# Kernel tuning notes

Hardware: AMD Instinct MI355X
Metric: run time of the kernel (lower is better)

Reference implementation:

```python
import jax, jax.numpy as jnp
import numpy as np

N, E = 50000, 1600000
IN, OUT, H = 128, 32, 2
NT, ET = 20, 4
ETE, EAE, ED = 16, 16, 16
SLOPE = 0.2  # conv_neg_slope


def setup_inputs() -> dict:
    key = jax.random.key(0)
    ks = jax.random.split(key, 11)
    d_att = 2 * OUT + ETE + EAE
    return dict(
        x=jax.random.normal(ks[0], (N, IN), jnp.float32),
        edge_index=jax.random.randint(ks[1], (2, E), 0, N),
        ntypes=jax.random.randint(ks[2], (N,), 0, NT),
        etypes=jax.random.randint(ks[3], (E,), 0, ET),
        eattr=jax.random.normal(ks[4], (E, ED), jnp.float32),
        het_W=jax.random.normal(ks[5], (NT, IN, OUT), jnp.float32) / np.sqrt(IN).astype(np.float32),
        het_b=jnp.zeros((NT, OUT), jnp.float32),
        etype_table=jax.random.normal(ks[6], (ET, ETE), jnp.float32),
        eattr_W=jax.random.normal(ks[7], (ED, EAE), jnp.float32) / np.sqrt(ED).astype(np.float32),
        att_W=jax.random.normal(ks[8], (d_att, H), jnp.float32) / np.sqrt(d_att).astype(np.float32),
        lin_W=jax.random.normal(ks[9], (OUT + EAE, OUT), jnp.float32) / np.sqrt(OUT + EAE).astype(np.float32),
    )


def _lrelu(v):
    return jax.nn.leaky_relu(v, SLOPE)


def _heat_conv(x, edge_index, ntypes, etypes, eattr,
               het_W, het_b, etype_table, eattr_W, att_W, lin_W):
    # HeteroLinear: node-type-conditioned linear transform (loop over 20 types,
    # avoids materializing a [N, IN, OUT] gathered-weight tensor)
    h = jnp.zeros((x.shape[0], het_W.shape[-1]), x.dtype)
    for t in range(het_W.shape[0]):
        h = h + jnp.where((ntypes == t)[:, None], x @ het_W[t] + het_b[t], 0.0)

    src, dst = edge_index[0], edge_index[1]
    ete = _lrelu(etype_table[etypes])        # [E, ETE] edge-type embedding
    ea = _lrelu(eattr @ eattr_W)             # [E, EAE] edge-attr embedding
    x_i = h[dst]                             # target node feats [E, OUT]
    x_j = h[src]                             # source node feats [E, OUT]

    feat = jnp.concatenate([x_i, x_j, ete, ea], axis=-1)
    alpha = _lrelu(feat @ att_W)             # [E, H] raw attention logits

    # softmax grouped by destination node, per head
    amax = jax.ops.segment_max(alpha, dst, num_segments=N)  # [N, H]
    alpha = jnp.exp(alpha - amax[dst])
    denom = jax.ops.segment_sum(alpha, dst, num_segments=N)  # [N, H]
    alpha = alpha / denom[dst]

    msg = jnp.concatenate([x_j, ea], axis=-1) @ lin_W        # [E, OUT]
    m = (msg[:, None, :] * alpha[:, :, None]).reshape(alpha.shape[0], H * OUT)
    out = jax.ops.segment_sum(m, dst, num_segments=N)        # [N, H*OUT]
    return out  # concat=True -> flattened heads


def reference(x, edge_index, ntypes, etypes, eattr,
              het_W, het_b, etype_table, eattr_W, att_W, lin_W):
    out = _heat_conv(x, edge_index, ntypes, etypes, eattr,
                     het_W, het_b, etype_table, eattr_W, att_W, lin_W)
    return jax.nn.relu(out)  # final activation in forward (eval mode: no dropout)
```

## Files before the change

kernel.cpp:

```cpp
#include <hip/hip_runtime.h>
#include <hip/hip_fp16.h>

#define NN 50000
#define EE 1600000
#define IN_F 128
#define SLOPE 0.2f
#define NB_SCAN 196
#define NSHARD 8

typedef _Float16 hf2 __attribute__((ext_vector_type(2)));

__global__ __launch_bounds__(256) void k_node(
    const float* __restrict__ x, const int* __restrict__ ntypes,
    const float* __restrict__ hetW, const float* __restrict__ hetb,
    const float* __restrict__ linW, const float* __restrict__ attW,
    float* __restrict__ hlin, float* __restrict__ auxS,
    float* __restrict__ auxD)
{
    __shared__ float sH[32 * 33];
    __shared__ float sLin[32 * 32];
    int tid = threadIdx.x;
    for (int i = tid; i < 1024; i += 256) sLin[i] = linW[i];

    int g = tid >> 3;
    int j = tid & 7;
    int n = blockIdx.x * 32 + g;
    int nc = n < NN ? n : NN - 1;
    int t = ntypes[nc];
    const float* W = hetW + (size_t)t * (IN_F * 32);
    const float4* xr = (const float4*)(x + (size_t)nc * IN_F);

    float4 acc = ((const float4*)(hetb + t * 32))[j];
    #pragma unroll 4
    for (int c = 0; c < 32; ++c) {
        float4 xv = xr[c];
        const float* Wr = W + (4 * c) * 32 + 4 * j;
        float4 w0 = *(const float4*)(Wr);
        float4 w1 = *(const float4*)(Wr + 32);
        float4 w2 = *(const float4*)(Wr + 64);
        float4 w3 = *(const float4*)(Wr + 96);
        acc.x += xv.x * w0.x + xv.y * w1.x + xv.z * w2.x + xv.w * w3.x;
        acc.y += xv.x * w0.y + xv.y * w1.y + xv.z * w2.y + xv.w * w3.y;
        acc.z += xv.x * w0.z + xv.y * w1.z + xv.z * w2.z + xv.w * w3.z;
        acc.w += xv.x * w0.w + xv.y * w1.w + xv.z * w2.w + xv.w * w3.w;
    }
    sH[g * 33 + 4 * j + 0] = acc.x;
    sH[g * 33 + 4 * j + 1] = acc.y;
    sH[g * 33 + 4 * j + 2] = acc.z;
    sH[g * 33 + 4 * j + 3] = acc.w;
    __syncthreads();

    int o = tid & 31;
    #pragma unroll
    for (int pass = 0; pass < 4; ++pass) {
        int g2 = (tid >> 5) + 8 * pass;
        int n2 = blockIdx.x * 32 + g2;
        if (n2 >= NN) break;
        float accl = 0.0f;
        #pragma unroll
        for (int k = 0; k < 32; ++k)
            accl += sH[g2 * 33 + k] * sLin[k * 32 + o];
        hlin[(size_t)n2 * 32 + o] = accl;

        float hv = sH[g2 * 33 + o];
        float p0 = hv * attW[o * 2],        p1 = hv * attW[o * 2 + 1];
        float p2 = hv * attW[(32 + o) * 2], p3 = hv * attW[(32 + o) * 2 + 1];
        #pragma unroll
        for (int m = 16; m >= 1; m >>= 1) {
            p0 += __shfl_xor(p0, m, 32);
            p1 += __shfl_xor(p1, m, 32);
            p2 += __shfl_xor(p2, m, 32);
            p3 += __shfl_xor(p3, m, 32);
        }
        if (o == 0) {
            auxD[n2 * 2] = p0; auxD[n2 * 2 + 1] = p1;
            auxS[n2 * 2] = p2; auxS[n2 * 2 + 1] = p3;
        }
    }
}

__global__ __launch_bounds__(256) void k_count(
    const int* __restrict__ dst, int* __restrict__ cnt8,
    unsigned* __restrict__ rankpack)
{
    int e = blockIdx.x * 256 + threadIdx.x;
    int d = dst[e];
    unsigned xcc;
    asm volatile("s_getreg_b32 %0, hwreg(HW_REG_XCC_ID)" : "=s"(xcc));
    int sh = xcc & (NSHARD - 1);
    int lr = atomicAdd(&cnt8[sh * NN + d], 1);
    rankpack[e] = ((unsigned)lr << 3) | (unsigned)sh;
}

__global__ __launch_bounds__(256) void k_scanA(
    const int* __restrict__ cnt8, int* __restrict__ offsets,
    int* __restrict__ bsum, int* __restrict__ sb8)
{
    __shared__ int s[256];
    int t = threadIdx.x;
    int i = blockIdx.x * 256 + t;
    int tot = 0;
    if (i < NN) {
        int pre = 0;
        #pragma unroll
        for (int sh = 0; sh < NSHARD; ++sh) {
            int c = cnt8[sh * NN + i];
            sb8[sh * NN + i] = pre;
            pre += c;
        }
        tot = pre;
    }
    s[t] = tot;
    __syncthreads();
    for (int off = 1; off < 256; off <<= 1) {
        int v = (t >= off) ? s[t - off] : 0;
        __syncthreads();
        s[t] += v;
        __syncthreads();
    }
    if (i < NN) offsets[i] = s[t] - tot;
    if (t == 255) bsum[blockIdx.x] = s[255];
}

__global__ __launch_bounds__(256) void k_scanB(
    const int* __restrict__ bsum, int* __restrict__ bbase,
    const float* __restrict__ etab, const float* __restrict__ attW,
    float* __restrict__ etedot)
{
    __shared__ int s[256];
    int t = threadIdx.x;
    if (t < 8) {
        int et = t >> 1, hh = t & 1;
        float acc = 0.0f;
        for (int k = 0; k < 16; ++k) {
            float v = etab[et * 16 + k];
            v = v > 0.0f ? v : SLOPE * v;
            acc += v * attW[(64 + k) * 2 + hh];
        }
        etedot[t] = acc;
    }
    int c = (t < NB_SCAN) ? bsum[t] : 0;
    s[t] = c;
    __syncthreads();
    for (int off = 1; off < 256; off <<= 1) {
        int v = (t >= off) ? s[t - off] : 0;
        __syncthreads();
        s[t] += v;
        __syncthreads();
    }
    if (t < NB_SCAN) bbase[t] = s[t] - c;
}

__global__ __launch_bounds__(256) void k_scanC(
    int* __restrict__ offsets, const int* __restrict__ bbase,
    int* __restrict__ sb8)
{
    int t = threadIdx.x;
    int i = blockIdx.x * 256 + t;
    if (i < NN) {
        int v = offsets[i] + bbase[blockIdx.x];
        offsets[i] = v;
        #pragma unroll
        for (int sh = 0; sh < NSHARD; ++sh)
            sb8[sh * NN + i] += v;
    }
    if (i == 0) offsets[NN] = EE;
}

__global__ __launch_bounds__(256) void k_pre6(
    const int* __restrict__ srcp, const int* __restrict__ dstp,
    const int* __restrict__ etypes, const float* __restrict__ eattr,
    const float* __restrict__ eaW, const float* __restrict__ attW,
    const float* __restrict__ etedot, const float* __restrict__ auxS,
    const float* __restrict__ auxD, const unsigned* __restrict__ rankpack,
    const int* __restrict__ sb8, float4* __restrict__ recBuf)
{
    int e = blockIdx.x * 256 + threadIdx.x;
    int s = srcp[e], d = dstp[e], et = etypes[e];
    unsigned rp = rankpack[e];
    int slot = sb8[(size_t)(rp & 7) * NN + d] + (int)(rp >> 3);

    float attr[16];
    {
        const float4* ap = (const float4*)(eattr + (size_t)e * 16);
        #pragma unroll
        for (int q = 0; q < 4; ++q) {
            float4 v = ap[q];
            attr[4*q+0] = v.x; attr[4*q+1] = v.y;
            attr[4*q+2] = v.z; attr[4*q+3] = v.w;
        }
    }
    float ea[16];
    #pragma unroll
    for (int j = 0; j < 16; ++j) {
        float acc = 0.0f;
        #pragma unroll
        for (int k = 0; k < 16; ++k) acc += attr[k] * eaW[k * 16 + j];
        ea[j] = acc > 0.0f ? acc : SLOPE * acc;
    }

    float2 aD = ((const float2*)auxD)[d];
    float2 aS = ((const float2*)auxS)[s];
    float2 eD = ((const float2*)etedot)[et];
    float al0 = aD.x + aS.x + eD.x;
    float al1 = aD.y + aS.y + eD.y;
    #pragma unroll
    for (int j = 0; j < 16; ++j) {
        al0 += ea[j] * attW[(80 + j) * 2];
        al1 += ea[j] * attW[(80 + j) * 2 + 1];
    }
    al0 = al0 > 0.0f ? al0 : SLOPE * al0;
    al1 = al1 > 0.0f ? al1 : SLOPE * al1;
    float p0 = __expf(al0), p1 = __expf(al1);

    __half2 eh[8];
    #pragma unroll
    for (int q = 0; q < 8; ++q)
        eh[q] = __floats2half2_rn(ea[2*q], ea[2*q+1]);

    float4* P = recBuf + (size_t)slot * 4;
    P[0] = ((const float4*)eh)[0];
    P[1] = ((const float4*)eh)[1];
    union { float4 v; int i[4]; float f[4]; } mu;
    mu.i[0] = s; mu.f[1] = p0; mu.f[2] = p1; mu.i[3] = 0;
    P[2] = mu.v;
    P[3] = make_float4(0.f, 0.f, 0.f, 0.f);
}

__global__ __launch_bounds__(256) void k_gather5(
    const int* __restrict__ offsets, const float4* __restrict__ recBuf,
    const float* __restrict__ hlin, const float* __restrict__ linW,
    float* __restrict__ out)
{
    int tid = blockIdx.x * 256 + threadIdx.x;
    int n = tid >> 6;
    int lane = threadIdx.x & 63;
    if (n >= NN) return;
    int o = lane & 31, hh = lane >> 5, j = o & 15;

    int s0 = __builtin_amdgcn_readfirstlane(offsets[n]);
    int s1 = __builtin_amdgcn_readfirstlane(offsets[n + 1]);

    const char* base = (const char*)recBuf;
    float accm = 0.0f, accp = 0.0f, wacc = 0.0f;

    int slot = s0;
    for (; slot + 3 < s1; slot += 4) {
        const char* r0 = base + ((size_t)(slot + 0) << 6);
        const char* r1 = base + ((size_t)(slot + 1) << 6);
        const char* r2 = base + ((size_t)(slot + 2) << 6);
        const char* r3 = base + ((size_t)(slot + 3) << 6);
        int4 m0 = *(const int4*)(r0 + 32);
        int4 m1 = *(const int4*)(r1 + 32);
        int4 m2 = *(const int4*)(r2 + 32);
        int4 m3 = *(const int4*)(r3 + 32);
        float e0 = __half2float(*(const __half*)(r0 + 2 * j));
        float e1 = __half2float(*(const __half*)(r1 + 2 * j));
        float e2 = __half2float(*(const __half*)(r2 + 2 * j));
        float e3 = __half2float(*(const __half*)(r3 + 2 * j));
        float hv0 = hlin[(size_t)m0.x * 32 + o];
        float hv1 = hlin[(size_t)m1.x * 32 + o];
        float hv2 = hlin[(size_t)m2.x * 32 + o];
        float hv3 = hlin[(size_t)m3.x * 32 + o];
        float p0 = __int_as_float(hh ? m0.z : m0.y);
        float p1 = __int_as_float(hh ? m1.z : m1.y);
        float p2 = __int_as_float(hh ? m2.z : m2.y);
        float p3 = __int_as_float(hh ? m3.z : m3.y);
        accm += p0 * hv0;
        accm += p1 * hv1;
        accm += p2 * hv2;
        accm += p3 * hv3;
        wacc += p0 * e0;
        wacc += p1 * e1;
        wacc += p2 * e2;
        wacc += p3 * e3;
        accp += (p0 + p1) + (p2 + p3);
    }
    for (; slot < s1; ++slot) {
        const char* r = base + ((size_t)slot << 6);
        int4 m = *(const int4*)(r + 32);
        float e = __half2float(*(const __half*)(r + 2 * j));
        float hv = hlin[(size_t)m.x * 32 + o];
        float p = __int_as_float(hh ? m.z : m.y);
        accm += p * hv;
        wacc += p * e;
        accp += p;
    }

    float elin = 0.0f;
    int bsel = lane & 32;
    #pragma unroll
    for (int jj = 0; jj < 16; ++jj) {
        float wv = __shfl(wacc, bsel | jj, 64);
        elin += wv * linW[(32 + jj) * 32 + o];
    }
    float num = accm + elin;
    float v = accp > 0.0f ? num / accp : 0.0f;
    out[(size_t)n * 64 + lane] = v > 0.0f ? v : 0.0f;
}

extern "C" void kernel_launch(void* const* d_in, const int* in_sizes, int n_in,
                              void* d_out, int out_size, void* d_ws, size_t ws_size,
                              hipStream_t stream)
{
    const float* x      = (const float*)d_in[0];
    const int*   eidx   = (const int*)  d_in[1];
    const int*   ntypes = (const int*)  d_in[2];
    const int*   etypes = (const int*)  d_in[3];
    const float* eattr  = (const float*)d_in[4];
    const float* hetW   = (const float*)d_in[5];
    const float* hetb   = (const float*)d_in[6];
    const float* etab   = (const float*)d_in[7];
    const float* eaW    = (const float*)d_in[8];
    const float* attW   = (const float*)d_in[9];
    const float* linW   = (const float*)d_in[10];
    float* out = (float*)d_out;

    char* ws = (char*)d_ws;
    size_t off = 0;
    auto alloc = [&](size_t bytes) {
        char* p = ws + off;
        off = (off + bytes + 255) & ~(size_t)255;
        return p;
    };
    float*    hlin     = (float*)   alloc((size_t)NN * 32 * sizeof(float));
    float*    auxS     = (float*)   alloc((size_t)NN * 2 * sizeof(float));
    float*    auxD     = (float*)   alloc((size_t)NN * 2 * sizeof(float));
    float*    etedot   = (float*)   alloc(8 * sizeof(float));
    int*      cnt8     = (int*)     alloc((size_t)NSHARD * NN * sizeof(int));
    int*      offsets  = (int*)     alloc(((size_t)NN + 1) * sizeof(int));
    int*      sb8      = (int*)     alloc((size_t)NSHARD * NN * sizeof(int));
    unsigned* rankpack = (unsigned*)alloc((size_t)EE * sizeof(unsigned));
    int*      bsum     = (int*)     alloc(256 * sizeof(int));
    int*      bbase    = (int*)     alloc(256 * sizeof(int));
    float4*   recBuf   = (float4*)  alloc((size_t)EE * 64);
    (void)ws_size;

    const int* srcp = eidx;
    const int* dstp = eidx + EE;

    hipMemsetAsync(cnt8, 0, (size_t)NSHARD * NN * sizeof(int), stream);

    k_node<<<(NN + 31) / 32, 256, 0, stream>>>(x, ntypes, hetW, hetb, linW,
                                               attW, hlin, auxS, auxD);
    k_count<<<EE / 256, 256, 0, stream>>>(dstp, cnt8, rankpack);
    k_scanA<<<NB_SCAN, 256, 0, stream>>>(cnt8, offsets, bsum, sb8);
    k_scanB<<<1, 256, 0, stream>>>(bsum, bbase, etab, attW, etedot);
    k_scanC<<<NB_SCAN, 256, 0, stream>>>(offsets, bbase, sb8);
    k_pre6<<<EE / 256, 256, 0, stream>>>(srcp, dstp, etypes, eattr, eaW, attW,
                                         etedot, auxS, auxD, rankpack, sb8,
                                         recBuf);
    k_gather5<<<(NN * 64 + 255) / 256, 256, 0, stream>>>(offsets, recBuf,
                                                         hlin, linW, out);
}
```

Baseline: 464.6 us.

## Fuse node transform with edge counting and store projected node features in fp16

The node HeteroLinear kernel and the per-destination atomic counting kernel become one launch. Every fifth block does node work and the other blocks do edge counting, so the compute-bound and atomic-bound work can overlap and one launch is saved. The lin_W-projected node features (hlin) are now written and read as fp16, which halves the bytes of the random per-edge gathers in the final aggregation kernel. The cost is reduced precision on the node message features.

Result: faster. 454.3 us (-2.2%).

```diff
diff --git a/kernel.cpp b/kernel.cpp
--- a/kernel.cpp
+++ b/kernel.cpp
@@ -7,24 +7,42 @@
 #define SLOPE 0.2f
 #define NB_SCAN 196
 #define NSHARD 8
+#define NB_NODE 1563
+#define NB_CNT  6250
+#define NB_FUSE (NB_NODE + NB_CNT)
 
 typedef _Float16 hf2 __attribute__((ext_vector_type(2)));
 
-__global__ __launch_bounds__(256) void k_node(
+__global__ __launch_bounds__(256) void k_node_count(
     const float* __restrict__ x, const int* __restrict__ ntypes,
     const float* __restrict__ hetW, const float* __restrict__ hetb,
     const float* __restrict__ linW, const float* __restrict__ attW,
-    float* __restrict__ hlin, float* __restrict__ auxS,
-    float* __restrict__ auxD)
-{
+    __half* __restrict__ hlinH, float* __restrict__ auxS,
+    float* __restrict__ auxD,
+    const int* __restrict__ dst, int* __restrict__ cnt8,
+    unsigned* __restrict__ rankpack)
+{
+    int b = blockIdx.x;
+    int tid = threadIdx.x;
+    if (b % 5 != 0) {
+        int cid = b - b / 5 - 1;
+        int e = cid * 256 + tid;
+        int d = dst[e];
+        unsigned xcc;
+        asm volatile("s_getreg_b32 %0, hwreg(HW_REG_XCC_ID)" : "=s"(xcc));
+        int sh = xcc & (NSHARD - 1);
+        int lr = atomicAdd(&cnt8[sh * NN + d], 1);
+        rankpack[e] = ((unsigned)lr << 3) | (unsigned)sh;
+        return;
+    }
+    int nb = b / 5;
     __shared__ float sH[32 * 33];
     __shared__ float sLin[32 * 32];
-    int tid = threadIdx.x;
     for (int i = tid; i < 1024; i += 256) sLin[i] = linW[i];
 
     int g = tid >> 3;
     int j = tid & 7;
-    int n = blockIdx.x * 32 + g;
+    int n = nb * 32 + g;
     int nc = n < NN ? n : NN - 1;
     int t = ntypes[nc];
     const float* W = hetW + (size_t)t * (IN_F * 32);
@@ -54,13 +72,13 @@
     #pragma unroll
     for (int pass = 0; pass < 4; ++pass) {
         int g2 = (tid >> 5) + 8 * pass;
-        int n2 = blockIdx.x * 32 + g2;
+        int n2 = nb * 32 + g2;
         if (n2 >= NN) break;
         float accl = 0.0f;
         #pragma unroll
         for (int k = 0; k < 32; ++k)
             accl += sH[g2 * 33 + k] * sLin[k * 32 + o];
-        hlin[(size_t)n2 * 32 + o] = accl;
+        hlinH[(size_t)n2 * 32 + o] = __float2half_rn(accl);
 
         float hv = sH[g2 * 33 + o];
         float p0 = hv * attW[o * 2],        p1 = hv * attW[o * 2 + 1];
@@ -77,19 +95,6 @@
             auxS[n2 * 2] = p2; auxS[n2 * 2 + 1] = p3;
         }
     }
-}
-
-__global__ __launch_bounds__(256) void k_count(
-    const int* __restrict__ dst, int* __restrict__ cnt8,
-    unsigned* __restrict__ rankpack)
-{
-    int e = blockIdx.x * 256 + threadIdx.x;
-    int d = dst[e];
-    unsigned xcc;
-    asm volatile("s_getreg_b32 %0, hwreg(HW_REG_XCC_ID)" : "=s"(xcc));
-    int sh = xcc & (NSHARD - 1);
-    int lr = atomicAdd(&cnt8[sh * NN + d], 1);
-    rankpack[e] = ((unsigned)lr << 3) | (unsigned)sh;
 }
 
 __global__ __launch_bounds__(256) void k_scanA(
@@ -227,9 +232,9 @@
     P[3] = make_float4(0.f, 0.f, 0.f, 0.f);
 }
 
-__global__ __launch_bounds__(256) void k_gather5(
+__global__ __launch_bounds__(256) void k_gather6(
     const int* __restrict__ offsets, const float4* __restrict__ recBuf,
-    const float* __restrict__ hlin, const float* __restrict__ linW,
+    const __half* __restrict__ hlinH, const float* __restrict__ linW,
     float* __restrict__ out)
 {
     int tid = blockIdx.x * 256 + threadIdx.x;
@@ -258,10 +263,10 @@
         float e1 = __half2float(*(const __half*)(r1 + 2 * j));
         float e2 = __half2float(*(const __half*)(r2 + 2 * j));
         float e3 = __half2float(*(const __half*)(r3 + 2 * j));
-        float hv0 = hlin[(size_t)m0.x * 32 + o];
-        float hv1 = hlin[(size_t)m1.x * 32 + o];
-        float hv2 = hlin[(size_t)m2.x * 32 + o];
-        float hv3 = hlin[(size_t)m3.x * 32 + o];
+        float hv0 = __half2float(hlinH[(size_t)m0.x * 32 + o]);
+        float hv1 = __half2float(hlinH[(size_t)m1.x * 32 + o]);
+        float hv2 = __half2float(hlinH[(size_t)m2.x * 32 + o]);
+        float hv3 = __half2float(hlinH[(size_t)m3.x * 32 + o]);
         float p0 = __int_as_float(hh ? m0.z : m0.y);
         float p1 = __int_as_float(hh ? m1.z : m1.y);
         float p2 = __int_as_float(hh ? m2.z : m2.y);
@@ -280,7 +285,7 @@
         const char* r = base + ((size_t)slot << 6);
         int4 m = *(const int4*)(r + 32);
         float e = __half2float(*(const __half*)(r + 2 * j));
-        float hv = hlin[(size_t)m.x * 32 + o];
+        float hv = __half2float(hlinH[(size_t)m.x * 32 + o]);
         float p = __int_as_float(hh ? m.z : m.y);
         accm += p * hv;
         wacc += p * e;
@@ -323,7 +328,7 @@
         off = (off + bytes + 255) & ~(size_t)255;
         return p;
     };
-    float*    hlin     = (float*)   alloc((size_t)NN * 32 * sizeof(float));
+    __half*   hlinH    = (__half*)  alloc((size_t)NN * 32 * sizeof(__half));
     float*    auxS     = (float*)   alloc((size_t)NN * 2 * sizeof(float));
     float*    auxD     = (float*)   alloc((size_t)NN * 2 * sizeof(float));
     float*    etedot   = (float*)   alloc(8 * sizeof(float));
@@ -341,15 +346,15 @@
 
     hipMemsetAsync(cnt8, 0, (size_t)NSHARD * NN * sizeof(int), stream);
 
-    k_node<<<(NN + 31) / 32, 256, 0, stream>>>(x, ntypes, hetW, hetb, linW,
-                                               attW, hlin, auxS, auxD);
-    k_count<<<EE / 256, 256, 0, stream>>>(dstp, cnt8, rankpack);
+    k_node_count<<<NB_FUSE, 256, 0, stream>>>(x, ntypes, hetW, hetb, linW,
+                                              attW, hlinH, auxS, auxD,
+                                              dstp, cnt8, rankpack);
     k_scanA<<<NB_SCAN, 256, 0, stream>>>(cnt8, offsets, bsum, sb8);
     k_scanB<<<1, 256, 0, stream>>>(bsum, bbase, etab, attW, etedot);
     k_scanC<<<NB_SCAN, 256, 0, stream>>>(offsets, bbase, sb8);
     k_pre6<<<EE / 256, 256, 0, stream>>>(srcp, dstp, etypes, eattr, eaW, attW,
                                          etedot, auxS, auxD, rankpack, sb8,
                                          recBuf);
-    k_gather5<<<(NN * 64 + 255) / 256, 256, 0, stream>>>(offsets, recBuf,
-                                                         hlin, linW, out);
-}
+    k_gather6<<<(NN * 64 + 255) / 256, 256, 0, stream>>>(offsets, recBuf,
+                                                         hlinH, linW, out);
+}
```
